# Kernel tuning notes

Hardware: AMD Instinct MI355X
Metric: run time of the kernel (lower is better)

## Reference

```python
import jax, jax.numpy as jnp
import numpy as np

N = 50000      # nodes
E = 400000     # directed edges (self-loops added inside reference, per PyG default)
DIN = 256
DH = 32
HEADS = 8
DOUT = 40
SLOPE = 0.2    # GATv2Conv negative_slope default


def _gatv2_layer(x, src, dst, Wl, bl, Wr, br, att, bias, heads, out_ch):
    """One GATv2Conv (concat=True). x:[n,din], src/dst:[e], att:[heads,out_ch]."""
    n = x.shape[0]
    xl = (x @ Wl + bl).reshape(n, heads, out_ch)   # source transform
    xr = (x @ Wr + br).reshape(n, heads, out_ch)   # target transform
    e = jax.nn.leaky_relu(xl[src] + xr[dst], SLOPE)          # [e, H, C]
    s = jnp.einsum('ehc,hc->eh', e, att)                     # per-edge attention logits
    smax = jax.ops.segment_max(s, dst, num_segments=n)       # stable softmax over in-edges
    ex = jnp.exp(s - smax[dst])
    denom = jax.ops.segment_sum(ex, dst, num_segments=n)
    alpha = ex / denom[dst]                                  # [e, H]
    out = jax.ops.segment_sum(alpha[:, :, None] * xl[src], dst, num_segments=n)
    return out.reshape(n, heads * out_ch) + bias


def setup_inputs() -> dict:
    key = jax.random.key(0)
    ks = jax.random.split(key, 8)
    def gl(k, shape, fan_in):
        return jax.random.normal(k, shape, jnp.float32) * np.float32(1.0 / np.sqrt(fan_in))
    return {
        'x': jax.random.normal(ks[0], (N, DIN), jnp.float32),
        'edge_index': jax.random.randint(ks[1], (2, E), 0, N, jnp.int32),
        'W1l': gl(ks[2], (DIN, HEADS * DH), DIN),
        'b1l': jnp.zeros((HEADS * DH,), jnp.float32),
        'W1r': gl(ks[3], (DIN, HEADS * DH), DIN),
        'b1r': jnp.zeros((HEADS * DH,), jnp.float32),
        'att1': gl(ks[4], (HEADS, DH), DH),
        'bias1': jnp.zeros((HEADS * DH,), jnp.float32),
        'W2l': gl(ks[5], (HEADS * DH, DOUT), HEADS * DH),
        'b2l': jnp.zeros((DOUT,), jnp.float32),
        'W2r': gl(ks[6], (HEADS * DH, DOUT), HEADS * DH),
        'b2r': jnp.zeros((DOUT,), jnp.float32),
        'att2': gl(ks[7], (1, DOUT), DOUT),
        'bias2': jnp.zeros((DOUT,), jnp.float32),
    }


def reference(x, edge_index, W1l, b1l, W1r, b1r, att1, bias1,
              W2l, b2l, W2r, b2r, att2, bias2):
    n = x.shape[0]
    loop = jnp.arange(n, dtype=edge_index.dtype)  # add_self_loops=True (PyG default)
    src = jnp.concatenate([edge_index[0], loop])
    dst = jnp.concatenate([edge_index[1], loop])
    # eval mode: F.dropout is identity; normalization='none' -> Identity
    h = _gatv2_layer(x, src, dst, W1l, b1l, W1r, b1r, att1, bias1, HEADS, DH)
    h = jax.nn.elu(h)
    out = _gatv2_layer(h, src, dst, W2l, b2l, W2r, b2r, att2, bias2, 1, DOUT)
    return jax.nn.log_softmax(out, axis=1)
```

## Files before the change

### kernel.cpp

```cpp
#include <hip/hip_runtime.h>
#include <math.h>

#define NODES 50000
#define NEDGE 400000
#define ETOT  450000
#define DIN   256
#define C1    256
#define C2    40
#define SCAN_NB ((NODES + 255) / 256)
#define CSRCAP  600064

typedef __attribute__((ext_vector_type(8))) short bfrag;
typedef __attribute__((ext_vector_type(4))) float facc;

#define GPTR(p) (const __attribute__((address_space(1))) unsigned int*)(p)
#define LPTR(p) (__attribute__((address_space(3))) unsigned int*)(p)

static __device__ __forceinline__ float bitsf(unsigned int x) {
    float f;
    __builtin_memcpy(&f, &x, 4);
    return f;
}
static __device__ __forceinline__ unsigned short f2bf(float f) {
    unsigned int x;
    __builtin_memcpy(&x, &f, 4);
    unsigned int r = x + 0x7fffu + ((x >> 16) & 1u);
    return (unsigned short)(r >> 16);
}
static __device__ __forceinline__ float fexp2(float x) {
#if __has_builtin(__builtin_amdgcn_exp2f)
    return __builtin_amdgcn_exp2f(x);
#else
    return exp2f(x);
#endif
}

__global__ __launch_bounds__(256)
void cvt_bf16(const float* __restrict__ in, unsigned short* __restrict__ out, int n8) {
    int i = blockIdx.x * 256 + threadIdx.x;
    if (i >= n8) return;
    const float4* p = (const float4*)in + (size_t)i * 2;
    float4 u0 = p[0], u1 = p[1];
    bfrag pk;
    pk[0] = (short)f2bf(u0.x); pk[1] = (short)f2bf(u0.y);
    pk[2] = (short)f2bf(u0.z); pk[3] = (short)f2bf(u0.w);
    pk[4] = (short)f2bf(u1.x); pk[5] = (short)f2bf(u1.y);
    pk[6] = (short)f2bf(u1.z); pk[7] = (short)f2bf(u1.w);
    *(bfrag*)(out + (size_t)i * 8) = pk;
}

__global__ void count_kernel(const int* __restrict__ dstRow, int* __restrict__ cnt) {
    int e = blockIdx.x * blockDim.x + threadIdx.x;
    if (e >= ETOT) return;
    int d = (e < NEDGE) ? dstRow[e] : (e - NEDGE);
    atomicAdd(&cnt[d], 1);
}

__global__ __launch_bounds__(256)
void scan_blk(const int* __restrict__ cnt, int* __restrict__ off, int* __restrict__ blkTot) {
    __shared__ int buf[256];
    const int t = threadIdx.x;
    const int i = blockIdx.x * 256 + t;
    int v = (i < NODES) ? ((cnt[i] + 3) & ~3) : 0;
    buf[t] = v;
    __syncthreads();
    #pragma unroll
    for (int d = 1; d < 256; d <<= 1) {
        int add = (t >= d) ? buf[t - d] : 0;
        __syncthreads();
        buf[t] += add;
        __syncthreads();
    }
    if (i < NODES) off[i] = buf[t] - v;
    if (t == 255) blkTot[blockIdx.x] = buf[255];
}

__global__ __launch_bounds__(256)
void scan_top(const int* __restrict__ blkTot, int* __restrict__ blkOff, int* __restrict__ offEnd) {
    __shared__ int buf[256];
    const int t = threadIdx.x;
    int v = (t < SCAN_NB) ? blkTot[t] : 0;
    buf[t] = v;
    __syncthreads();
    #pragma unroll
    for (int d = 1; d < 256; d <<= 1) {
        int add = (t >= d) ? buf[t - d] : 0;
        __syncthreads();
        buf[t] += add;
        __syncthreads();
    }
    if (t < SCAN_NB) blkOff[t] = buf[t] - v;
    if (t == 255) *offEnd = buf[255];
}

__global__ __launch_bounds__(256)
void scan_fix(int* __restrict__ off, int* __restrict__ wrk, const int* __restrict__ blkOff) {
    const int i = blockIdx.x * 256 + threadIdx.x;
    if (i < NODES) {
        int v = off[i] + blkOff[blockIdx.x];
        off[i] = v;
        wrk[i] = v;
    }
}

__global__ void place_kernel(const int* __restrict__ srcRow, const int* __restrict__ dstRow,
                             int* __restrict__ wrk, int* __restrict__ csr) {
    int e = blockIdx.x * blockDim.x + threadIdx.x;
    if (e >= ETOT) return;
    int d, s;
    if (e < NEDGE) { d = dstRow[e]; s = srcRow[e]; }
    else           { d = e - NEDGE; s = d; }
    int slot = atomicAdd(&wrk[d], 1);
    csr[slot] = s;
}

__global__ void prep_w(const float* __restrict__ Wl, const float* __restrict__ Wr,
                       unsigned short* __restrict__ Wt, int K, int Nhalf) {
    int idx = blockIdx.x * 256 + threadIdx.x;
    int n = idx / K;
    int k = idx - n * K;
    if (n >= 2 * Nhalf) return;
    float v = (n < Nhalf) ? Wl[(size_t)k * Nhalf + n] : Wr[(size_t)k * Nhalf + (n - Nhalf)];
    Wt[idx] = f2bf(v);
}

#define GBM 128
#define GBN 128
#define GBK 32

template<typename OUTT, bool SWZ>
__global__ __launch_bounds__(256)
void mfma_gemm(const unsigned short* __restrict__ Ab, const unsigned short* __restrict__ Bt,
               const float* __restrict__ bl, const float* __restrict__ br,
               OUTT* __restrict__ Cl, OUTT* __restrict__ Cr,
               int M, int K, int Nrows, int Nhalf, int nbnShift)
{
    __shared__ __align__(16) unsigned short As[2][GBM * GBK];
    __shared__ __align__(16) unsigned short Bs[2][GBN * GBK];

    const int tid  = threadIdx.x;
    const int lane = tid & 63;
    const int w    = tid >> 6;
    const int wr   = w >> 1;
    const int wc   = w & 1;

    int tile;
    if constexpr (SWZ) {
        const int nwg = gridDim.x;
        const int q = nwg >> 3, r = nwg & 7;
        const int xcd = blockIdx.x & 7;
        const int idx = blockIdx.x >> 3;
        tile = (xcd < r ? xcd * (q + 1) : r * (q + 1) + (xcd - r) * q) + idx;
    } else {
        tile = blockIdx.x;
    }
    const int bx   = tile >> nbnShift;
    const int by   = tile & ((1 << nbnShift) - 1);
    const int row0 = bx * GBM;
    const int col0 = by * GBN;

    facc acc[4][4];
    #pragma unroll
    for (int i = 0; i < 4; ++i)
        #pragma unroll
        for (int j = 0; j < 4; ++j) {
            facc z = {0.f, 0.f, 0.f, 0.f};
            acc[i][j] = z;
        }

    const int rA  = lane >> 2;
    const int kgA = (lane & 3) ^ ((rA >> 1) & 3);

    #define STAGE(bufi, k0)                                                     \
    {                                                                           \
        _Pragma("unroll")                                                       \
        for (int p = 0; p < 2; ++p) {                                           \
            const int chunk = p * 4 + w;                                        \
            const int r_loc = chunk * 16 + rA;                                  \
            const int ga = min(row0 + r_loc, M - 1);                            \
            __builtin_amdgcn_global_load_lds(                                   \
                GPTR(Ab + (size_t)ga * K + (k0) + kgA * 8),                     \
                LPTR(&As[bufi][chunk * 512]), 16, 0, 0);                        \
            const int gb = min(col0 + r_loc, Nrows - 1);                        \
            __builtin_amdgcn_global_load_lds(                                   \
                GPTR(Bt + (size_t)gb * K + (k0) + kgA * 8),                     \
                LPTR(&Bs[bufi][chunk * 512]), 16, 0, 0);                        \
        }                                                                       \
    }

    const int fr    = lane & 15;
    const int sRead = (lane >> 4) ^ ((fr >> 1) & 3);
    const int nt    = K / GBK;

    STAGE(0, 0);
    for (int t = 0; t < nt; ++t) {
        const int cur = t & 1;
        if (t + 1 < nt) {
            STAGE(cur ^ 1, (t + 1) * GBK);
            asm volatile("s_waitcnt vmcnt(4)" ::: "memory");
        } else {
            asm volatile("s_waitcnt vmcnt(0)" ::: "memory");
        }
        __builtin_amdgcn_s_barrier();
        __builtin_amdgcn_sched_barrier(0);

        bfrag af[4], bfv[4];
        #pragma unroll
        for (int mi = 0; mi < 4; ++mi)
            af[mi] = *(const bfrag*)(&As[cur][(wr * 64 + mi * 16 + fr) * 32 + sRead * 8]);
        #pragma unroll
        for (int ni = 0; ni < 4; ++ni)
            bfv[ni] = *(const bfrag*)(&Bs[cur][(wc * 64 + ni * 16 + fr) * 32 + sRead * 8]);
        #pragma unroll
        for (int mi = 0; mi < 4; ++mi)
            #pragma unroll
            for (int ni = 0; ni < 4; ++ni)
                acc[mi][ni] = __builtin_amdgcn_mfma_f32_16x16x32_bf16(
                    af[mi], bfv[ni], acc[mi][ni], 0, 0, 0);

        __builtin_amdgcn_s_barrier();
    }
    #undef STAGE

    #pragma unroll
    for (int mi = 0; mi < 4; ++mi) {
        const int rbase = row0 + wr * 64 + mi * 16 + ((lane >> 4) << 2);
        #pragma unroll
        for (int ni = 0; ni < 4; ++ni) {
            const int col = col0 + wc * 64 + ni * 16 + (lane & 15);
            #pragma unroll
            for (int rg = 0; rg < 4; ++rg) {
                int r = rbase + rg;
                if (r >= M) continue;
                float v = acc[mi][ni][rg];
                if (col < Nhalf) {
                    v += bl[col];
                    if constexpr (sizeof(OUTT) == 2)
                        Cl[(size_t)r * Nhalf + col] = (OUTT)f2bf(v);
                    else
                        Cl[(size_t)r * Nhalf + col] = (OUTT)v;
                } else if (col < 2 * Nhalf) {
                    int c2 = col - Nhalf;
                    v += br[c2];
                    if constexpr (sizeof(OUTT) == 2)
                        Cr[(size_t)r * Nhalf + c2] = (OUTT)f2bf(v);
                    else
                        Cr[(size_t)r * Nhalf + c2] = (OUTT)v;
                }
            }
        }
    }
}

__global__ __launch_bounds__(256)
void fused_l1(const int* __restrict__ off, const int* __restrict__ deg,
              const int* __restrict__ csr, const unsigned short* __restrict__ xl,
              const unsigned short* __restrict__ xr, const float* __restrict__ att,
              const float* __restrict__ bias, unsigned short* __restrict__ hout)
{
    const int lane = threadIdx.x & 63;
    const int n    = blockIdx.x * 4 + (threadIdx.x >> 6);
    if (n >= NODES) return;

    const int a  = __builtin_amdgcn_readfirstlane(off[n]);
    const int dn = __builtin_amdgcn_readfirstlane(deg[n]);
    const int np = (dn + 3) & ~3;

    const uint2 xrn = *(const uint2*)(xr + (size_t)n * C1 + lane * 4);
    const float xr0 = bitsf(xrn.x << 16), xr1 = bitsf(xrn.x & 0xffff0000u);
    const float xr2 = bitsf(xrn.y << 16), xr3 = bitsf(xrn.y & 0xffff0000u);
    const float4 wv = *(const float4*)(att + lane * 4);
    const float L2E = 1.4426950408889634f;
    const float w6_0 = wv.x * (0.6f * L2E), w4_0 = wv.x * (0.4f * L2E);
    const float w6_1 = wv.y * (0.6f * L2E), w4_1 = wv.y * (0.4f * L2E);
    const float w6_2 = wv.z * (0.6f * L2E), w4_2 = wv.z * (0.4f * L2E);
    const float w6_3 = wv.w * (0.6f * L2E), w4_3 = wv.w * (0.4f * L2E);

    float m = -INFINITY, d = 0.f;
    float a0 = 0.f, a1 = 0.f, a2 = 0.f, a3 = 0.f;

    uint2 R[4];
    {
        const int4 s4 = *(const int4*)(csr + a);
        R[0] = *(const uint2*)(xl + (size_t)s4.x * C1 + lane * 4);
        R[1] = *(const uint2*)(xl + (size_t)s4.y * C1 + lane * 4);
        R[2] = *(const uint2*)(xl + (size_t)s4.z * C1 + lane * 4);
        R[3] = *(const uint2*)(xl + (size_t)s4.w * C1 + lane * 4);
    }

    for (int i = 0; i < np; i += 4) {
        uint2 Rn[4];
        const int nx = (i + 4 < np) ? (i + 4) : i;
        {
            const int4 s4 = *(const int4*)(csr + a + nx);
            Rn[0] = *(const uint2*)(xl + (size_t)s4.x * C1 + lane * 4);
            Rn[1] = *(const uint2*)(xl + (size_t)s4.y * C1 + lane * 4);
            Rn[2] = *(const uint2*)(xl + (size_t)s4.z * C1 + lane * 4);
            Rn[3] = *(const uint2*)(xl + (size_t)s4.w * C1 + lane * 4);
        }

        float x0[4], x1[4], x2[4], x3[4], p[4];
        #pragma unroll
        for (int k = 0; k < 4; ++k) {
            x0[k] = bitsf(R[k].x << 16);
            x1[k] = bitsf(R[k].x & 0xffff0000u);
            x2[k] = bitsf(R[k].y << 16);
            x3[k] = bitsf(R[k].y & 0xffff0000u);
            const float v0 = x0[k] + xr0, v1 = x1[k] + xr1;
            const float v2 = x2[k] + xr2, v3 = x3[k] + xr3;
            float pp;
            pp = w6_0 * v0;
            pp = fmaf(w4_0, fabsf(v0), pp);
            pp = fmaf(w6_1, v1, pp);
            pp = fmaf(w4_1, fabsf(v1), pp);
            pp = fmaf(w6_2, v2, pp);
            pp = fmaf(w4_2, fabsf(v2), pp);
            pp = fmaf(w6_3, v3, pp);
            pp = fmaf(w4_3, fabsf(v3), pp);
            pp += __shfl_xor(pp, 1);
            pp += __shfl_xor(pp, 2);
            pp += __shfl_xor(pp, 4);
            p[k] = (i + k < dn) ? pp : -INFINITY;
        }

        const float pm = fmaxf(fmaxf(p[0], p[1]), fmaxf(p[2], p[3]));
        if (__any(pm > m + 8.f)) {
            #pragma unroll
            for (int k = 0; k < 4; ++k) {
                const float mN = fmaxf(m, p[k]);
                const float sc = fexp2(m - mN);
                const float wg = fexp2(p[k] - mN);
                m = mN;
                d = fmaf(d, sc, wg);
                a0 = fmaf(wg, x0[k], a0 * sc);
                a1 = fmaf(wg, x1[k], a1 * sc);
                a2 = fmaf(wg, x2[k], a2 * sc);
                a3 = fmaf(wg, x3[k], a3 * sc);
            }
        } else {
            #pragma unroll
            for (int k = 0; k < 4; ++k) {
                const float wg = fexp2(p[k] - m);
                d += wg;
                a0 = fmaf(wg, x0[k], a0);
                a1 = fmaf(wg, x1[k], a1);
                a2 = fmaf(wg, x2[k], a2);
                a3 = fmaf(wg, x3[k], a3);
            }
        }

        #pragma unroll
        for (int k = 0; k < 4; ++k) R[k] = Rn[k];
    }

    const float inv = 1.f / d;
    const float4 bv = *(const float4*)(bias + lane * 4);
    float v0 = fmaf(a0, inv, bv.x), v1 = fmaf(a1, inv, bv.y);
    float v2 = fmaf(a2, inv, bv.z), v3 = fmaf(a3, inv, bv.w);
    v0 = v0 > 0.f ? v0 : (fexp2(v0 * L2E) - 1.f);
    v1 = v1 > 0.f ? v1 : (fexp2(v1 * L2E) - 1.f);
    v2 = v2 > 0.f ? v2 : (fexp2(v2 * L2E) - 1.f);
    v3 = v3 > 0.f ? v3 : (fexp2(v3 * L2E) - 1.f);
    uint2 o;
    o.x = (unsigned int)f2bf(v0) | ((unsigned int)f2bf(v1) << 16);
    o.y = (unsigned int)f2bf(v2) | ((unsigned int)f2bf(v3) << 16);
    *(uint2*)(hout + (size_t)n * C1 + lane * 4) = o;
}

__global__ __launch_bounds__(256)
void fused_l2(const int* __restrict__ off, const int* __restrict__ deg,
              const int* __restrict__ csr, const float* __restrict__ h2l,
              const float* __restrict__ h2r, const float* __restrict__ att,
              const float* __restrict__ bias, float* __restrict__ out)
{
    const int lane = threadIdx.x & 63;
    const int n    = blockIdx.x * 4 + (threadIdx.x >> 6);
    if (n >= NODES) return;
    const int l8 = lane & 7;
    const int g  = lane >> 3;

    const int a  = __builtin_amdgcn_readfirstlane(off[n]);
    const int dn = __builtin_amdgcn_readfirstlane(deg[n]);
    const float L2E = 1.4426950408889634f;

    float w6[5], w4[5], xr[5];
    #pragma unroll
    for (int j = 0; j < 5; ++j) {
        const int c = l8 + 8 * j;
        const float w = att[c];
        w6[j] = w * (0.6f * L2E);
        w4[j] = w * (0.4f * L2E);
        xr[j] = h2r[(size_t)n * C2 + c];
    }

    float m = -INFINITY, dl = 0.f;
    float acc[5] = {0.f, 0.f, 0.f, 0.f, 0.f};

    float R[5];
    {
        const int src = csr[a + g];
        const float* row = h2l + (size_t)src * C2 + l8;
        #pragma unroll
        for (int j = 0; j < 5; ++j) R[j] = row[8 * j];
    }

    for (int c0 = 0; c0 < dn; c0 += 8) {
        float Rn[5];
        {
            const int nx = (c0 + 8 < dn) ? (c0 + 8) : c0;
            const int src = csr[a + nx + g];
            const float* row = h2l + (size_t)src * C2 + l8;
            #pragma unroll
            for (int j = 0; j < 5; ++j) Rn[j] = row[8 * j];
        }

        const int idx = c0 + g;
        float p = 0.f;
        #pragma unroll
        for (int j = 0; j < 5; ++j) {
            const float v = R[j] + xr[j];
            p = fmaf(w6[j], v, p);
            p = fmaf(w4[j], fabsf(v), p);
        }
        p += __shfl_xor(p, 1);
        p += __shfl_xor(p, 2);
        p += __shfl_xor(p, 4);
        if (idx >= dn) p = -INFINITY;

        if (__any(p > m + 8.f)) {
            float pm = p;
            pm = fmaxf(pm, __shfl_xor(pm, 8));
            pm = fmaxf(pm, __shfl_xor(pm, 16));
            pm = fmaxf(pm, __shfl_xor(pm, 32));
            const float mN = fmaxf(m, pm);
            const float sc = fexp2(m - mN);
            const float wg = fexp2(p - mN);
            m = mN;
            dl = fmaf(dl, sc, wg);
            #pragma unroll
            for (int j = 0; j < 5; ++j) acc[j] = fmaf(wg, R[j], acc[j] * sc);
        } else {
            const float wg = fexp2(p - m);
            dl += wg;
            #pragma unroll
            for (int j = 0; j < 5; ++j) acc[j] = fmaf(wg, R[j], acc[j]);
        }

        #pragma unroll
        for (int j = 0; j < 5; ++j) R[j] = Rn[j];
    }

    #pragma unroll
    for (int o = 8; o < 64; o <<= 1) {
        dl += __shfl_xor(dl, o);
        #pragma unroll
        for (int j = 0; j < 5; ++j) acc[j] += __shfl_xor(acc[j], o);
    }

    const float inv = 1.f / dl;
    float v[5];
    float mx = -INFINITY;
    #pragma unroll
    for (int j = 0; j < 5; ++j) {
        v[j] = fmaf(acc[j], inv, bias[l8 + 8 * j]);
        mx = fmaxf(mx, v[j]);
    }
    mx = fmaxf(mx, __shfl_xor(mx, 1));
    mx = fmaxf(mx, __shfl_xor(mx, 2));
    mx = fmaxf(mx, __shfl_xor(mx, 4));
    float s = 0.f;
    #pragma unroll
    for (int j = 0; j < 5; ++j) s += fexp2((v[j] - mx) * L2E);
    s += __shfl_xor(s, 1);
    s += __shfl_xor(s, 2);
    s += __shfl_xor(s, 4);
    const float lg = logf(s);
    if (g == 0) {
        #pragma unroll
        for (int j = 0; j < 5; ++j)
            out[(size_t)n * C2 + l8 + 8 * j] = v[j] - mx - lg;
    }
}

extern "C" void kernel_launch(void* const* d_in, const int* in_sizes, int n_in,
                              void* d_out, int out_size, void* d_ws, size_t ws_size,
                              hipStream_t stream)
{
    const float* x     = (const float*)d_in[0];
    const int*   ei    = (const int*)  d_in[1];
    const float* W1l   = (const float*)d_in[2];
    const float* b1l   = (const float*)d_in[3];
    const float* W1r   = (const float*)d_in[4];
    const float* b1r   = (const float*)d_in[5];
    const float* att1  = (const float*)d_in[6];
    const float* bias1 = (const float*)d_in[7];
    const float* W2l   = (const float*)d_in[8];
    const float* b2l   = (const float*)d_in[9];
    const float* W2r   = (const float*)d_in[10];
    const float* b2r   = (const float*)d_in[11];
    const float* att2  = (const float*)d_in[12];
    const float* bias2 = (const float*)d_in[13];
    float* out = (float*)d_out;

    float* ws = (float*)d_ws;
    unsigned short* xl1 = (unsigned short*)ws;
    unsigned short* xr1 = (unsigned short*)(ws + 6400000);
    unsigned short* xb  = (unsigned short*)(ws + 12800000);
    int*   csr    = (int*)(ws + 19200000);
    int*   off    = csr + CSRCAP;
    int*   cnt    = off + (NODES + 1);
    int*   wrk    = cnt + NODES;
    int*   blkTot = wrk + NODES;
    int*   blkOff = blkTot + SCAN_NB;
    unsigned short* Wt1 = (unsigned short*)(ws + 19960000);
    unsigned short* Wt2 = (unsigned short*)(ws + 20030000);
    unsigned short* h = xr1;
    float* h2l = ws;
    float* h2r = ws + 2000000;

    const int* srcRow = ei;
    const int* dstRow = ei + NEDGE;

    hipMemsetAsync(cnt, 0, NODES * sizeof(int), stream);
    hipMemsetAsync(csr, 0, CSRCAP * sizeof(int), stream);
    count_kernel<<<(ETOT + 255) / 256, 256, 0, stream>>>(dstRow, cnt);
    scan_blk<<<SCAN_NB, 256, 0, stream>>>(cnt, off, blkTot);
    scan_top<<<1, 256, 0, stream>>>(blkTot, blkOff, off + NODES);
    scan_fix<<<SCAN_NB, 256, 0, stream>>>(off, wrk, blkOff);
    place_kernel<<<(ETOT + 255) / 256, 256, 0, stream>>>(srcRow, dstRow, wrk, csr);

    cvt_bf16<<<(NODES * DIN / 8 + 255) / 256, 256, 0, stream>>>(x, xb, NODES * DIN / 8);
    prep_w<<<(512 * 256 + 255) / 256, 256, 0, stream>>>(W1l, W1r, Wt1, DIN, C1);
    prep_w<<<(80 * 256 + 255) / 256, 256, 0, stream>>>(W2l, W2r, Wt2, C1, C2);

    mfma_gemm<unsigned short, true><<<((NODES + GBM - 1) / GBM) * 4, 256, 0, stream>>>(
        xb, Wt1, b1l, b1r, xl1, xr1, NODES, DIN, 2 * C1, C1, 2);
    fused_l1<<<(NODES + 3) / 4, 256, 0, stream>>>(off, cnt, csr, xl1, xr1, att1, bias1, h);

    mfma_gemm<float, false><<<(NODES + GBM - 1) / GBM, 256, 0, stream>>>(
        h, Wt2, b2l, b2r, h2l, h2r, NODES, C1, 2 * C2, C2, 0);
    fused_l2<<<(NODES + 3) / 4, 256, 0, stream>>>(off, cnt, csr, h2l, h2r, att2, bias2, out);
}
```

Measured before the change: 211.9 us.

## Deepen GEMM pipeline to four LDS stages and pack GAT math into float2 ops

New measurement: 219.4 us. 3.5% more time.

```diff
diff --git a/kernel.cpp b/kernel.cpp
--- a/kernel.cpp
+++ b/kernel.cpp
@@ -12,6 +12,7 @@
 
 typedef __attribute__((ext_vector_type(8))) short bfrag;
 typedef __attribute__((ext_vector_type(4))) float facc;
+typedef __attribute__((ext_vector_type(2))) float f32x2;
 
 #define GPTR(p) (const __attribute__((address_space(1))) unsigned int*)(p)
 #define LPTR(p) (__attribute__((address_space(3))) unsigned int*)(p)
@@ -33,6 +34,12 @@
 #else
     return exp2f(x);
 #endif
+}
+static __device__ __forceinline__ f32x2 vfma(f32x2 a, f32x2 b, f32x2 c) {
+    return __builtin_elementwise_fma(a, b, c);
+}
+static __device__ __forceinline__ f32x2 vabs(f32x2 a) {
+    return __builtin_elementwise_abs(a);
 }
 
 __global__ __launch_bounds__(256)
@@ -133,10 +140,10 @@
 void mfma_gemm(const unsigned short* __restrict__ Ab, const unsigned short* __restrict__ Bt,
                const float* __restrict__ bl, const float* __restrict__ br,
                OUTT* __restrict__ Cl, OUTT* __restrict__ Cr,
-               int M, int K, int Nrows, int Nhalf, int nbnShift)
+               int M, int Nrows, int Nhalf, int nbnShift)
 {
-    __shared__ __align__(16) unsigned short As[2][GBM * GBK];
-    __shared__ __align__(16) unsigned short Bs[2][GBN * GBK];
+    __shared__ __align__(16) unsigned short As[4][GBM * GBK];
+    __shared__ __align__(16) unsigned short Bs[4][GBN * GBK];
 
     const int tid  = threadIdx.x;
     const int lane = tid & 63;
@@ -170,6 +177,8 @@
 
     const int rA  = lane >> 2;
     const int kgA = (lane & 3) ^ ((rA >> 1) & 3);
+    const int fr    = lane & 15;
+    const int sRead = (lane >> 4) ^ ((fr >> 1) & 3);
 
     #define STAGE(bufi, k0)                                                     \
     {                                                                           \
@@ -179,47 +188,43 @@
             const int r_loc = chunk * 16 + rA;                                  \
             const int ga = min(row0 + r_loc, M - 1);                            \
             __builtin_amdgcn_global_load_lds(                                   \
-                GPTR(Ab + (size_t)ga * K + (k0) + kgA * 8),                     \
+                GPTR(Ab + (size_t)ga * 256 + (k0) + kgA * 8),                   \
                 LPTR(&As[bufi][chunk * 512]), 16, 0, 0);                        \
             const int gb = min(col0 + r_loc, Nrows - 1);                        \
             __builtin_amdgcn_global_load_lds(                                   \
-                GPTR(Bt + (size_t)gb * K + (k0) + kgA * 8),                     \
+                GPTR(Bt + (size_t)gb * 256 + (k0) + kgA * 8),                   \
                 LPTR(&Bs[bufi][chunk * 512]), 16, 0, 0);                        \
         }                                                                       \
     }
 
-    const int fr    = lane & 15;
-    const int sRead = (lane >> 4) ^ ((fr >> 1) & 3);
-    const int nt    = K / GBK;
-
-    STAGE(0, 0);
-    for (int t = 0; t < nt; ++t) {
-        const int cur = t & 1;
-        if (t + 1 < nt) {
-            STAGE(cur ^ 1, (t + 1) * GBK);
-            asm volatile("s_waitcnt vmcnt(4)" ::: "memory");
-        } else {
-            asm volatile("s_waitcnt vmcnt(0)" ::: "memory");
-        }
-        __builtin_amdgcn_s_barrier();
-        __builtin_amdgcn_sched_barrier(0);
-
-        bfrag af[4], bfv[4];
-        #pragma unroll
-        for (int mi = 0; mi < 4; ++mi)
-            af[mi] = *(const bfrag*)(&As[cur][(wr * 64 + mi * 16 + fr) * 32 + sRead * 8]);
-        #pragma unroll
-        for (int ni = 0; ni < 4; ++ni)
-            bfv[ni] = *(const bfrag*)(&Bs[cur][(wc * 64 + ni * 16 + fr) * 32 + sRead * 8]);
-        #pragma unroll
-        for (int mi = 0; mi < 4; ++mi)
-            #pragma unroll
-            for (int ni = 0; ni < 4; ++ni)
-                acc[mi][ni] = __builtin_amdgcn_mfma_f32_16x16x32_bf16(
-                    af[mi], bfv[ni], acc[mi][ni], 0, 0, 0);
-
-        __builtin_amdgcn_s_barrier();
-    }
+    #define KSTEP(T, WSTR)                                                      \
+    {                                                                           \
+        asm volatile("s_waitcnt vmcnt(" WSTR ")" ::: "memory");                 \
+        __builtin_amdgcn_s_barrier();                                           \
+        __builtin_amdgcn_sched_barrier(0);                                      \
+        constexpr int cur = (T) & 3;                                            \
+        bfrag af[4], bfv[4];                                                    \
+        _Pragma("unroll")                                                       \
+        for (int mi = 0; mi < 4; ++mi)                                          \
+            af[mi] = *(const bfrag*)(&As[cur][(wr * 64 + mi * 16 + fr) * 32 + sRead * 8]); \
+        _Pragma("unroll")                                                       \
+        for (int ni = 0; ni < 4; ++ni)                                          \
+            bfv[ni] = *(const bfrag*)(&Bs[cur][(wc * 64 + ni * 16 + fr) * 32 + sRead * 8]); \
+        _Pragma("unroll")                                                       \
+        for (int mi = 0; mi < 4; ++mi)                                          \
+            _Pragma("unroll")                                                   \
+            for (int ni = 0; ni < 4; ++ni)                                      \
+                acc[mi][ni] = __builtin_amdgcn_mfma_f32_16x16x32_bf16(          \
+                    af[mi], bfv[ni], acc[mi][ni], 0, 0, 0);                     \
+        if constexpr ((T) + 3 < 8) STAGE(((T) + 3) & 3, ((T) + 3) * GBK);       \
+    }
+
+    STAGE(0, 0 * GBK);
+    STAGE(1, 1 * GBK);
+    STAGE(2, 2 * GBK);
+    KSTEP(0, "8"); KSTEP(1, "8"); KSTEP(2, "8"); KSTEP(3, "8");
+    KSTEP(4, "8"); KSTEP(5, "8"); KSTEP(6, "4"); KSTEP(7, "0");
+    #undef KSTEP
     #undef STAGE
 
     #pragma unroll
@@ -267,17 +272,17 @@
     const int np = (dn + 3) & ~3;
 
     const uint2 xrn = *(const uint2*)(xr + (size_t)n * C1 + lane * 4);
-    const float xr0 = bitsf(xrn.x << 16), xr1 = bitsf(xrn.x & 0xffff0000u);
-    const float xr2 = bitsf(xrn.y << 16), xr3 = bitsf(xrn.y & 0xffff0000u);
+    const f32x2 xr01 = {bitsf(xrn.x << 16), bitsf(xrn.x & 0xffff0000u)};
+    const f32x2 xr23 = {bitsf(xrn.y << 16), bitsf(xrn.y & 0xffff0000u)};
     const float4 wv = *(const float4*)(att + lane * 4);
     const float L2E = 1.4426950408889634f;
-    const float w6_0 = wv.x * (0.6f * L2E), w4_0 = wv.x * (0.4f * L2E);
-    const float w6_1 = wv.y * (0.6f * L2E), w4_1 = wv.y * (0.4f * L2E);
-    const float w6_2 = wv.z * (0.6f * L2E), w4_2 = wv.z * (0.4f * L2E);
-    const float w6_3 = wv.w * (0.6f * L2E), w4_3 = wv.w * (0.4f * L2E);
+    const f32x2 w6a = {wv.x * (0.6f * L2E), wv.y * (0.6f * L2E)};
+    const f32x2 w4a = {wv.x * (0.4f * L2E), wv.y * (0.4f * L2E)};
+    const f32x2 w6b = {wv.z * (0.6f * L2E), wv.w * (0.6f * L2E)};
+    const f32x2 w4b = {wv.z * (0.4f * L2E), wv.w * (0.4f * L2E)};
 
     float m = -INFINITY, d = 0.f;
-    float a0 = 0.f, a1 = 0.f, a2 = 0.f, a3 = 0.f;
+    f32x2 ac01 = {0.f, 0.f}, ac23 = {0.f, 0.f};
 
     uint2 R[4];
     {
@@ -299,24 +304,19 @@
             Rn[3] = *(const uint2*)(xl + (size_t)s4.w * C1 + lane * 4);
         }
 
-        float x0[4], x1[4], x2[4], x3[4], p[4];
+        f32x2 x01[4], x23[4];
+        float p[4];
         #pragma unroll
         for (int k = 0; k < 4; ++k) {
-            x0[k] = bitsf(R[k].x << 16);
-            x1[k] = bitsf(R[k].x & 0xffff0000u);
-            x2[k] = bitsf(R[k].y << 16);
-            x3[k] = bitsf(R[k].y & 0xffff0000u);
-            const float v0 = x0[k] + xr0, v1 = x1[k] + xr1;
-            const float v2 = x2[k] + xr2, v3 = x3[k] + xr3;
-            float pp;
-            pp = w6_0 * v0;
-            pp = fmaf(w4_0, fabsf(v0), pp);
-            pp = fmaf(w6_1, v1, pp);
-            pp = fmaf(w4_1, fabsf(v1), pp);
-            pp = fmaf(w6_2, v2, pp);
-            pp = fmaf(w4_2, fabsf(v2), pp);
-            pp = fmaf(w6_3, v3, pp);
-            pp = fmaf(w4_3, fabsf(v3), pp);
+            x01[k] = {bitsf(R[k].x << 16), bitsf(R[k].x & 0xffff0000u)};
+            x23[k] = {bitsf(R[k].y << 16), bitsf(R[k].y & 0xffff0000u)};
+            const f32x2 v01 = x01[k] + xr01;
+            const f32x2 v23 = x23[k] + xr23;
+            f32x2 t2 = w6a * v01;
+            t2 = vfma(w4a, vabs(v01), t2);
+            t2 = vfma(w6b, v23, t2);
+            t2 = vfma(w4b, vabs(v23), t2);
+            float pp = t2.x + t2.y;
             pp += __shfl_xor(pp, 1);
             pp += __shfl_xor(pp, 2);
             pp += __shfl_xor(pp, 4);
@@ -332,20 +332,19 @@
                 const float wg = fexp2(p[k] - mN);
                 m = mN;
                 d = fmaf(d, sc, wg);
-                a0 = fmaf(wg, x0[k], a0 * sc);
-                a1 = fmaf(wg, x1[k], a1 * sc);
-                a2 = fmaf(wg, x2[k], a2 * sc);
-                a3 = fmaf(wg, x3[k], a3 * sc);
+                const f32x2 s2 = {sc, sc};
+                const f32x2 g2 = {wg, wg};
+                ac01 = vfma(g2, x01[k], ac01 * s2);
+                ac23 = vfma(g2, x23[k], ac23 * s2);
             }
         } else {
             #pragma unroll
             for (int k = 0; k < 4; ++k) {
                 const float wg = fexp2(p[k] - m);
                 d += wg;
-                a0 = fmaf(wg, x0[k], a0);
-                a1 = fmaf(wg, x1[k], a1);
-                a2 = fmaf(wg, x2[k], a2);
-                a3 = fmaf(wg, x3[k], a3);
+                const f32x2 g2 = {wg, wg};
+                ac01 = vfma(g2, x01[k], ac01);
+                ac23 = vfma(g2, x23[k], ac23);
             }
         }
 
@@ -355,8 +354,8 @@
 
     const float inv = 1.f / d;
     const float4 bv = *(const float4*)(bias + lane * 4);
-    float v0 = fmaf(a0, inv, bv.x), v1 = fmaf(a1, inv, bv.y);
-    float v2 = fmaf(a2, inv, bv.z), v3 = fmaf(a3, inv, bv.w);
+    float v0 = fmaf(ac01.x, inv, bv.x), v1 = fmaf(ac01.y, inv, bv.y);
+    float v2 = fmaf(ac23.x, inv, bv.z), v3 = fmaf(ac23.y, inv, bv.w);
     v0 = v0 > 0.f ? v0 : (fexp2(v0 * L2E) - 1.f);
     v1 = v1 > 0.f ? v1 : (fexp2(v1 * L2E) - 1.f);
     v2 = v2 > 0.f ? v2 : (fexp2(v2 * L2E) - 1.f);
@@ -534,10 +533,10 @@
     prep_w<<<(80 * 256 + 255) / 256, 256, 0, stream>>>(W2l, W2r, Wt2, C1, C2);
 
     mfma_gemm<unsigned short, true><<<((NODES + GBM - 1) / GBM) * 4, 256, 0, stream>>>(
-        xb, Wt1, b1l, b1r, xl1, xr1, NODES, DIN, 2 * C1, C1, 2);
+        xb, Wt1, b1l, b1r, xl1, xr1, NODES, 2 * C1, C1, 2);
     fused_l1<<<(NODES + 3) / 4, 256, 0, stream>>>(off, cnt, csr, xl1, xr1, att1, bias1, h);
 
     mfma_gemm<float, false><<<(NODES + GBM - 1) / GBM, 256, 0, stream>>>(
-        h, Wt2, b2l, b2r, h2l, h2r, NODES, C1, 2 * C2, C2, 0);
+        h, Wt2, b2l, b2r, h2l, h2r, NODES, 2 * C2, C2, 0);
     fused_l2<<<(NODES + 3) / 4, 256, 0, stream>>>(off, cnt, csr, h2l, h2r, att2, bias2, out);
 }
```

## Triple-buffer GEMM LDS staging with fully unrolled fixed-K loop

Applied to the files above, without the earlier changes.

Result: no change. 209.6 us (-1.1%).

```diff
diff --git a/kernel.cpp b/kernel.cpp
--- a/kernel.cpp
+++ b/kernel.cpp
@@ -133,10 +133,10 @@
 void mfma_gemm(const unsigned short* __restrict__ Ab, const unsigned short* __restrict__ Bt,
                const float* __restrict__ bl, const float* __restrict__ br,
                OUTT* __restrict__ Cl, OUTT* __restrict__ Cr,
-               int M, int K, int Nrows, int Nhalf, int nbnShift)
+               int M, int Nrows, int Nhalf, int nbnShift)
 {
-    __shared__ __align__(16) unsigned short As[2][GBM * GBK];
-    __shared__ __align__(16) unsigned short Bs[2][GBN * GBK];
+    __shared__ __align__(16) unsigned short As[3][GBM * GBK];
+    __shared__ __align__(16) unsigned short Bs[3][GBN * GBK];
 
     const int tid  = threadIdx.x;
     const int lane = tid & 63;
@@ -170,6 +170,8 @@
 
     const int rA  = lane >> 2;
     const int kgA = (lane & 3) ^ ((rA >> 1) & 3);
+    const int fr    = lane & 15;
+    const int sRead = (lane >> 4) ^ ((fr >> 1) & 3);
 
     #define STAGE(bufi, k0)                                                     \
     {                                                                           \
@@ -179,47 +181,42 @@
             const int r_loc = chunk * 16 + rA;                                  \
             const int ga = min(row0 + r_loc, M - 1);                            \
             __builtin_amdgcn_global_load_lds(                                   \
-                GPTR(Ab + (size_t)ga * K + (k0) + kgA * 8),                     \
+                GPTR(Ab + (size_t)ga * 256 + (k0) + kgA * 8),                   \
                 LPTR(&As[bufi][chunk * 512]), 16, 0, 0);                        \
             const int gb = min(col0 + r_loc, Nrows - 1);                        \
             __builtin_amdgcn_global_load_lds(                                   \
-                GPTR(Bt + (size_t)gb * K + (k0) + kgA * 8),                     \
+                GPTR(Bt + (size_t)gb * 256 + (k0) + kgA * 8),                   \
                 LPTR(&Bs[bufi][chunk * 512]), 16, 0, 0);                        \
         }                                                                       \
     }
 
-    const int fr    = lane & 15;
-    const int sRead = (lane >> 4) ^ ((fr >> 1) & 3);
-    const int nt    = K / GBK;
-
-    STAGE(0, 0);
-    for (int t = 0; t < nt; ++t) {
-        const int cur = t & 1;
-        if (t + 1 < nt) {
-            STAGE(cur ^ 1, (t + 1) * GBK);
-            asm volatile("s_waitcnt vmcnt(4)" ::: "memory");
-        } else {
-            asm volatile("s_waitcnt vmcnt(0)" ::: "memory");
-        }
-        __builtin_amdgcn_s_barrier();
-        __builtin_amdgcn_sched_barrier(0);
-
-        bfrag af[4], bfv[4];
-        #pragma unroll
-        for (int mi = 0; mi < 4; ++mi)
-            af[mi] = *(const bfrag*)(&As[cur][(wr * 64 + mi * 16 + fr) * 32 + sRead * 8]);
-        #pragma unroll
-        for (int ni = 0; ni < 4; ++ni)
-            bfv[ni] = *(const bfrag*)(&Bs[cur][(wc * 64 + ni * 16 + fr) * 32 + sRead * 8]);
-        #pragma unroll
-        for (int mi = 0; mi < 4; ++mi)
-            #pragma unroll
-            for (int ni = 0; ni < 4; ++ni)
-                acc[mi][ni] = __builtin_amdgcn_mfma_f32_16x16x32_bf16(
-                    af[mi], bfv[ni], acc[mi][ni], 0, 0, 0);
-
-        __builtin_amdgcn_s_barrier();
-    }
+    #define KSTEP(T, WSTR)                                                      \
+    {                                                                           \
+        asm volatile("s_waitcnt vmcnt(" WSTR ")" ::: "memory");                 \
+        __builtin_amdgcn_s_barrier();                                           \
+        __builtin_amdgcn_sched_barrier(0);                                      \
+        constexpr int cur = (T) % 3;                                            \
+        bfrag af[4], bfv[4];                                                    \
+        _Pragma("unroll")                                                       \
+        for (int mi = 0; mi < 4; ++mi)                                          \
+            af[mi] = *(const bfrag*)(&As[cur][(wr * 64 + mi * 16 + fr) * 32 + sRead * 8]); \
+        _Pragma("unroll")                                                       \
+        for (int ni = 0; ni < 4; ++ni)                                          \
+            bfv[ni] = *(const bfrag*)(&Bs[cur][(wc * 64 + ni * 16 + fr) * 32 + sRead * 8]); \
+        if constexpr ((T) + 2 < 8) STAGE(((T) + 2) % 3, ((T) + 2) * GBK);       \
+        _Pragma("unroll")                                                       \
+        for (int mi = 0; mi < 4; ++mi)                                          \
+            _Pragma("unroll")                                                   \
+            for (int ni = 0; ni < 4; ++ni)                                      \
+                acc[mi][ni] = __builtin_amdgcn_mfma_f32_16x16x32_bf16(          \
+                    af[mi], bfv[ni], acc[mi][ni], 0, 0, 0);                     \
+    }
+
+    STAGE(0, 0 * GBK);
+    STAGE(1, 1 * GBK);
+    KSTEP(0, "4"); KSTEP(1, "4"); KSTEP(2, "4"); KSTEP(3, "4");
+    KSTEP(4, "4"); KSTEP(5, "4"); KSTEP(6, "4"); KSTEP(7, "0");
+    #undef KSTEP
     #undef STAGE
 
     #pragma unroll
@@ -534,10 +531,10 @@
     prep_w<<<(80 * 256 + 255) / 256, 256, 0, stream>>>(W2l, W2r, Wt2, C1, C2);
 
     mfma_gemm<unsigned short, true><<<((NODES + GBM - 1) / GBM) * 4, 256, 0, stream>>>(
-        xb, Wt1, b1l, b1r, xl1, xr1, NODES, DIN, 2 * C1, C1, 2);
+        xb, Wt1, b1l, b1r, xl1, xr1, NODES, 2 * C1, C1, 2);
     fused_l1<<<(NODES + 3) / 4, 256, 0, stream>>>(off, cnt, csr, xl1, xr1, att1, bias1, h);
 
     mfma_gemm<float, false><<<(NODES + GBM - 1) / GBM, 256, 0, stream>>>(
-        h, Wt2, b2l, b2r, h2l, h2r, NODES, C1, 2 * C2, C2, 0);
+        h, Wt2, b2l, b2r, h2l, h2r, NODES, 2 * C2, C2, 0);
     fused_l2<<<(NODES + 3) / 4, 256, 0, stream>>>(off, cnt, csr, h2l, h2r, att2, bias2, out);
 }
```
